# Kernel optimization log

Hardware: AMD Instinct MI355X
Metric: run time of the kernel (lower is better)

## Reference

```python
import jax, jax.numpy as jnp
import numpy as np

N = 4096
D = 256
TAU = 0.8
LAM = 0.5
K0, K1 = 64, 128


def setup_inputs() -> dict:
    key = jax.random.key(0)
    ks = jax.random.split(key, 20)
    s = 1.0 / np.sqrt(D)
    pos = (jax.random.uniform(ks[3], (N, N)) < 0.01).astype(jnp.float32)
    pos = pos.at[jnp.arange(N), jnp.arange(N)].set(1.0)  # guarantee a positive per row
    return {
        'z_mp': jax.random.normal(ks[0], (N, D), jnp.float32),
        'z_sc': jax.random.normal(ks[1], (N, D), jnp.float32),
        'feat': jax.random.normal(ks[2], (N, D), jnp.float32),
        'pos': pos,
        'im2c0': jax.random.randint(ks[4], (N,), 0, K0, jnp.int32),
        'im2c1': jax.random.randint(ks[5], (N,), 0, K1, jnp.int32),
        'centroids0': jax.random.normal(ks[6], (K0, D), jnp.float32),
        'centroids1': jax.random.normal(ks[7], (K1, D), jnp.float32),
        'density0': jax.random.uniform(ks[8], (K0,), jnp.float32) + 0.5,
        'density1': jax.random.uniform(ks[9], (K1,), jnp.float32) + 0.5,
        'pW1': jax.random.normal(ks[10], (D, D), jnp.float32) * s * 1.414,
        'pb1': jnp.zeros((D,), jnp.float32),
        'pW2': jax.random.normal(ks[11], (D, D), jnp.float32) * s * 1.414,
        'pb2': jnp.zeros((D,), jnp.float32),
        'mW1': jax.random.normal(ks[12], (D, D), jnp.float32) * s,
        'mb1': jnp.zeros((D,), jnp.float32),
        'mW2': jax.random.normal(ks[13], (D, D), jnp.float32) * s,
        'mb2': jnp.zeros((D,), jnp.float32),
    }


def _mlp(x, W1, b1, W2, b2):
    # nn.Linear -> ELU -> nn.Linear (torch Linear: x @ W.T + b)
    return jax.nn.elu(x @ W1.T + b1) @ W2.T + b2


def _sim(z1, z2, tau):
    n1 = jnp.linalg.norm(z1, axis=-1, keepdims=True)
    n2 = jnp.linalg.norm(z2, axis=-1, keepdims=True)
    return jnp.exp((z1 @ z2.T) / (n1 @ n2.T) / tau)


def _nce(sim_matrix, pos):
    m = sim_matrix / (sim_matrix.sum(axis=1, keepdims=True) + 1e-8)
    return -jnp.log((m * pos).sum(axis=-1)).mean()


def _pocl(z_anchor, z, im2cs, centroids, densities):
    n = z_anchor.shape[0]
    # weight[a,b] = #levels where a,b share a cluster (original: coo @ coo.T summed)
    sames = [(c[:, None] == c[None, :]).astype(z.dtype) for c in im2cs]
    weight = sames[0] + sames[1]
    node_prototypes = jnp.zeros_like(z)
    loss = jnp.float32(0.0)
    for same, im2c, protos, dens in zip(sames, im2cs, centroids, densities):
        # original aliases weight_clus = weight, so masking accumulates in-place
        weight = weight * same
        c = (weight @ z) / weight.sum(axis=1)[:, None]
        node_prototypes = node_prototypes + 0.1 * c
        phi = dens[im2c]
        pos_p = jnp.exp((z_anchor * node_prototypes).sum(axis=1) / phi)
        neg_p = jnp.exp((z_anchor @ protos.T) / dens).mean(axis=1) * n
        loss = loss + (-jnp.log(pos_p / neg_p)).mean()
    return loss / len(im2cs)


def reference(z_mp, z_sc, feat, pos, im2c0, im2c1, centroids0, centroids1,
              density0, density1, pW1, pb1, pW2, pb2, mW1, mb1, mW2, mb2):
    z_proj_mp = _mlp(z_mp, pW1, pb1, pW2, pb2)
    z_proj_sc = _mlp(z_sc, pW1, pb1, pW2, pb2)
    m_mp2sc = _sim(z_proj_mp, z_proj_sc, TAU)
    lori_mp = _nce(m_mp2sc, pos)
    lori_sc = _nce(m_mp2sc.T, pos)
    proto_loss = _pocl(z_sc, z_mp, [im2c0, im2c1],
                       [centroids0, centroids1], [density0, density1])
    mp_intra = _mlp(z_mp, mW1, mb1, mW2, mb2)
    loss_intramp = _nce(_sim(mp_intra, mp_intra, 0.05), pos)
    proj_mp_feat = _mlp(z_mp, pW1, pb1, pW2, pb2)
    proj_feat = _mlp(feat, pW1, pb1, pW2, pb2)
    lori_mpfeat = _nce(_sim(proj_mp_feat, proj_feat, TAU), pos)
    lori_featmp = _nce(_sim(proj_feat, proj_mp_feat, TAU), pos)
    return (LAM * lori_mp + (1 - LAM) * lori_sc + 0.3 * loss_intramp
            + proto_loss + 0.01 * lori_mpfeat + 0.01 * lori_featmp)
```

## Files before the change

### kernel.cpp

```cpp
#include <hip/hip_runtime.h>
#include <math.h>


#define NROWS 4096
#define DIM   256
#define ND    ((size_t)NROWS * DIM)

typedef unsigned short u16;
typedef unsigned int   u32;
typedef unsigned long long u64;
typedef __attribute__((ext_vector_type(8))) short bf16x8;
typedef __attribute__((ext_vector_type(4))) float f32x4;

__device__ __forceinline__ u16 f2bf(float f) {
    u32 u = __float_as_uint(f);
    return (u16)((u + 0x7fffu + ((u >> 16) & 1u)) >> 16);
}
__device__ __forceinline__ float bf2f(u16 h) {
    return __uint_as_float(((u32)h) << 16);
}

__device__ __forceinline__ void gload16(const u16* g, u16* l) {
    __builtin_amdgcn_global_load_lds(
        (const __attribute__((address_space(1))) u32*)g,
        (__attribute__((address_space(3))) u32*)l, 16, 0, 0);
}

template<int ROWS>
__device__ __forceinline__ void stage_panel(const u16* P, int kk, u16* S, int tid) {
#pragma unroll
    for (int p = 0; p < ROWS / 64; ++p) {
        const int ch = p * 256 + tid, row = ch >> 2, seg = ch & 3;
        gload16(P + (size_t)row * DIM + kk + seg * 8, &S[ch * 8]);
    }
}

__device__ __forceinline__ void wait_lgkm0() {
    asm volatile("s_waitcnt lgkmcnt(0)" ::: "memory");
    __builtin_amdgcn_sched_barrier(0);
}
template<int N> __device__ __forceinline__ void wait_vm() {
    if constexpr (N == 0)      asm volatile("s_waitcnt vmcnt(0)" ::: "memory");
    else if constexpr (N == 3) asm volatile("s_waitcnt vmcnt(3)" ::: "memory");
    else if constexpr (N == 4) asm volatile("s_waitcnt vmcnt(4)" ::: "memory");
}

__device__ __forceinline__ float rowsum16(float v) {
    v += __int_as_float(__builtin_amdgcn_update_dpp(0, __float_as_int(v), 0x118, 0xf, 0xf, true));
    v += __int_as_float(__builtin_amdgcn_update_dpp(0, __float_as_int(v), 0x114, 0xf, 0xf, true));
    v += __int_as_float(__builtin_amdgcn_update_dpp(0, __float_as_int(v), 0x112, 0xf, 0xf, true));
    v += __int_as_float(__builtin_amdgcn_update_dpp(0, __float_as_int(v), 0x111, 0xf, 0xf, true));
    return v;
}

struct PreArgs {
    const float* in0; const float* in1; const float* in2;
    const float* w0; const float* w1; const float* w2; const float* w3;
    const float* c0; const float* c1;
    const float* pos; const float* z_mp;
    const int* im0; const int* im1;
};
__global__ __launch_bounds__(256) void fused_pre(PreArgs p,
                                                 u16* __restrict__ INb,
                                                 u16* __restrict__ Wb,
                                                 u16* __restrict__ CB,
                                                 u64* __restrict__ bits,
                                                 float* __restrict__ S01,
                                                 float* __restrict__ cnt01)
{
    const int b = blockIdx.x, tid = threadIdx.x;
    if (b < 3072) {
        const int z = b >> 10;
        const float* s = z == 0 ? p.in0 : (z == 1 ? p.in1 : p.in2);
        const int i = (b & 1023) * 256 + tid;
        const float4 v = ((const float4*)s)[i];
        ushort4 o;
        o.x = f2bf(v.x); o.y = f2bf(v.y); o.z = f2bf(v.z); o.w = f2bf(v.w);
        ((ushort4*)(INb + (size_t)z * ND))[i] = o;
    } else if (b < 3328) {
        const int q = b - 3072, wi = q >> 6;
        const float* s = wi == 0 ? p.w0 : (wi == 1 ? p.w1 : (wi == 2 ? p.w2 : p.w3));
        const int i = (q & 63) * 256 + tid;
        const float4 v = ((const float4*)s)[i];
        ushort4 o;
        o.x = f2bf(v.x); o.y = f2bf(v.y); o.z = f2bf(v.z); o.w = f2bf(v.w);
        ((ushort4*)(Wb + (size_t)wi * 65536))[i] = o;
    } else if (b < 3376) {
        const int i = (b - 3328) * 256 + tid;
        const float4 v = (i < 4096) ? ((const float4*)p.c0)[i]
                                    : ((const float4*)p.c1)[i - 4096];
        ushort4 o;
        o.x = f2bf(v.x); o.y = f2bf(v.y); o.z = f2bf(v.z); o.w = f2bf(v.w);
        ((ushort4*)CB)[i] = o;
    } else if (b < 7472) {
        const int i = b - 3376;
        const int w = tid >> 6, l = tid & 63;
#pragma unroll
        for (int c = 0; c < 16; ++c) {
            const int j = c * 256 + w * 64 + l;
            const float v = p.pos[(size_t)i * NROWS + j];
            const u64 m = __ballot(v != 0.f);
            if (l == 0) bits[(size_t)i * 64 + c * 4 + w] = m;
        }
    } else {
        const int r = b - 7472;
        const int pp = p.im0[r] * 128 + p.im1[r];
        atomicAdd(&S01[(size_t)pp * DIM + tid], p.z_mp[(size_t)r * DIM + tid]);
        if (tid == 0) atomicAdd(&cnt01[pp], 1.f);
    }
}

template<int ACT, int REMAP, int SQ>
__device__ __forceinline__ void mlp_body(int bx, int by, u16* lds, int tid,
                                         const u16* __restrict__ IN,
                                         const u16* __restrict__ Wp,
                                         const u16* __restrict__ Wm,
                                         const float* __restrict__ bp,
                                         const float* __restrict__ bm,
                                         u16* __restrict__ OUT,
                                         float* __restrict__ SS)
{
    u16* As = lds;
    u16* Bs = lds + 3 * 2048;
    const bool intra = by >= 192;
    const int arow = (REMAP && intra) ? (by - 192) * 64 : by * 64;
    const u16* A = IN + (size_t)arow * DIM;
    const u16* B = (intra ? Wm : Wp) + (size_t)(bx * 128) * DIM;
    const float* bias = intra ? bm : bp;
    const int l = tid & 63, w = tid >> 6, wr = w >> 1, wc = w & 1;
    const int lr = l & 15, lk = l >> 4;

    f32x4 acc[2][4] = {};
    stage_panel<64>(A, 0, As, tid);
    stage_panel<128>(B, 0, Bs, tid);
    stage_panel<64>(A, 32, As + 2048, tid);
    stage_panel<128>(B, 32, Bs + 4096, tid);
    wait_vm<3>();
    __builtin_amdgcn_s_barrier();
#pragma unroll
    for (int t = 0; t < 8; ++t) {
        bf16x8 a[2], b[4];
#pragma unroll
        for (int mi = 0; mi < 2; ++mi)
            a[mi] = *(const bf16x8*)&As[(t % 3) * 2048 + (wr * 32 + mi * 16 + lr) * 32 + lk * 8];
#pragma unroll
        for (int ni = 0; ni < 4; ++ni)
            b[ni] = *(const bf16x8*)&Bs[(t % 3) * 4096 + (wc * 64 + ni * 16 + lr) * 32 + lk * 8];
        if (t < 6) {
            stage_panel<64>(A, (t + 2) * 32, As + ((t + 2) % 3) * 2048, tid);
            stage_panel<128>(B, (t + 2) * 32, Bs + ((t + 2) % 3) * 4096, tid);
        }
        wait_lgkm0();
#pragma unroll
        for (int mi = 0; mi < 2; ++mi)
#pragma unroll
            for (int ni = 0; ni < 4; ++ni)
                acc[mi][ni] = __builtin_amdgcn_mfma_f32_16x16x32_bf16(a[mi], b[ni], acc[mi][ni], 0, 0, 0);
        if (t < 6)      { wait_vm<3>(); __builtin_amdgcn_s_barrier(); }
        else if (t < 7) { wait_vm<0>(); __builtin_amdgcn_s_barrier(); }
    }

    const int j0 = bx * 128;
    float bv[4];
#pragma unroll
    for (int ni = 0; ni < 4; ++ni) bv[ni] = bias[j0 + wc * 64 + ni * 16 + lr];
#pragma unroll
    for (int mi = 0; mi < 2; ++mi)
#pragma unroll
        for (int r = 0; r < 4; ++r) {
            const int row = by * 64 + wr * 32 + mi * 16 + lk * 4 + r;
            float v4[4], sq = 0.f;
#pragma unroll
            for (int ni = 0; ni < 4; ++ni) {
                float v = acc[mi][ni][r] + bv[ni];
                if (ACT) v = v > 0.f ? v : expm1f(v);
                v4[ni] = v;
                sq += v * v;
            }
            if (SQ) {
                sq = rowsum16(sq);
                if (lr == 15) atomicAdd(&SS[row], sq);
            }
#pragma unroll
            for (int ni = 0; ni < 4; ++ni)
                OUT[(size_t)row * DIM + j0 + wc * 64 + ni * 16 + lr] = f2bf(v4[ni]);
        }
}

__device__ __forceinline__ void gcent_body(int bx, int by, u16* lds, int tid,
                                           const u16* __restrict__ Zb,
                                           const u16* __restrict__ CB,
                                           float* __restrict__ G)
{
    u16* As = lds;
    u16* Bs = lds + 3 * 4096;
    const int i0 = by * 128, j0 = bx * 64;
    const u16* A = Zb + (size_t)i0 * DIM;
    const u16* B = CB + (size_t)j0 * DIM;
    const int l = tid & 63, w = tid >> 6, wr = w >> 1, wc = w & 1;
    const int lr = l & 15, lk = l >> 4;

    f32x4 acc[4][2] = {};
    stage_panel<128>(A, 0, As, tid);
    stage_panel<64>(B, 0, Bs, tid);
    stage_panel<128>(A, 32, As + 4096, tid);
    stage_panel<64>(B, 32, Bs + 2048, tid);
    wait_vm<3>();
    __builtin_amdgcn_s_barrier();
#pragma unroll
    for (int t = 0; t < 8; ++t) {
        bf16x8 a[4], b[2];
#pragma unroll
        for (int mi = 0; mi < 4; ++mi)
            a[mi] = *(const bf16x8*)&As[(t % 3) * 4096 + (wr * 64 + mi * 16 + lr) * 32 + lk * 8];
#pragma unroll
        for (int ni = 0; ni < 2; ++ni)
            b[ni] = *(const bf16x8*)&Bs[(t % 3) * 2048 + (wc * 32 + ni * 16 + lr) * 32 + lk * 8];
        if (t < 6) {
            stage_panel<128>(A, (t + 2) * 32, As + ((t + 2) % 3) * 4096, tid);
            stage_panel<64>(B, (t + 2) * 32, Bs + ((t + 2) % 3) * 2048, tid);
        }
        wait_lgkm0();
#pragma unroll
        for (int mi = 0; mi < 4; ++mi)
#pragma unroll
            for (int ni = 0; ni < 2; ++ni)
                acc[mi][ni] = __builtin_amdgcn_mfma_f32_16x16x32_bf16(a[mi], b[ni], acc[mi][ni], 0, 0, 0);
        if (t < 6)      { wait_vm<3>(); __builtin_amdgcn_s_barrier(); }
        else if (t < 7) { wait_vm<0>(); __builtin_amdgcn_s_barrier(); }
    }

#pragma unroll
    for (int mi = 0; mi < 4; ++mi)
#pragma unroll
        for (int r = 0; r < 4; ++r) {
            const int row = i0 + wr * 64 + mi * 16 + lk * 4 + r;
#pragma unroll
            for (int ni = 0; ni < 2; ++ni)
                G[(size_t)row * 192 + j0 + wc * 32 + ni * 16 + lr] = acc[mi][ni][r];
        }
}

__device__ __forceinline__ void pocl_body(int blk, int tid,
                                          const float* __restrict__ z_sc,
                                          const int* __restrict__ i0a,
                                          const int* __restrict__ i1a,
                                          const float* __restrict__ S0,
                                          const float* __restrict__ S01,
                                          const float* __restrict__ cnt0,
                                          const float* __restrict__ cnt01,
                                          const float* __restrict__ G,
                                          const float* __restrict__ d0,
                                          const float* __restrict__ d1,
                                          float* __restrict__ L1,
                                          float* __restrict__ L2)
{
    const int w = tid >> 6, l = tid & 63;
    const int a = blk * 4 + w;
    const int k0 = i0a[a], k1 = i1a[a];
    const int p = k0 * 128 + k1;
    const float n0 = cnt0[k0], n01 = cnt01[p];
    const float inv1 = 1.f / (n0 + n01), inv2 = 1.f / n01;
    const float4 s0  = *(const float4*)&S0[(size_t)k0 * DIM + l * 4];
    const float4 s01 = *(const float4*)&S01[(size_t)p * DIM + l * 4];
    const float4 zd  = *(const float4*)&z_sc[(size_t)a * DIM + l * 4];

    float dot1 = 0.f, dot2 = 0.f;
    {
        const float c1x = (s0.x + s01.x) * inv1, c2x = s01.x * inv2;
        const float c1y = (s0.y + s01.y) * inv1, c2y = s01.y * inv2;
        const float c1z = (s0.z + s01.z) * inv1, c2z = s01.z * inv2;
        const float c1w = (s0.w + s01.w) * inv1, c2w = s01.w * inv2;
        dot1 = zd.x * c1x + zd.y * c1y + zd.z * c1z + zd.w * c1w;
        dot2 = zd.x * (c1x + c2x) + zd.y * (c1y + c2y) + zd.z * (c1z + c2z) + zd.w * (c1w + c2w);
    }
    dot1 *= 0.1f; dot2 *= 0.1f;
#pragma unroll
    for (int m = 1; m < 64; m <<= 1) {
        dot1 += __shfl_xor(dot1, m);
        dot2 += __shfl_xor(dot2, m);
    }

    const float x0 = G[(size_t)a * 192 + l] / d0[l];
    float M0 = x0;
#pragma unroll
    for (int m = 1; m < 64; m <<= 1) M0 = fmaxf(M0, __shfl_xor(M0, m));
    float e0 = __expf(x0 - M0);
#pragma unroll
    for (int m = 1; m < 64; m <<= 1) e0 += __shfl_xor(e0, m);

    const float x1a = G[(size_t)a * 192 + 64 + l] / d1[l];
    const float x1b = G[(size_t)a * 192 + 128 + l] / d1[64 + l];
    float M1 = fmaxf(x1a, x1b);
#pragma unroll
    for (int m = 1; m < 64; m <<= 1) M1 = fmaxf(M1, __shfl_xor(M1, m));
    float e1 = __expf(x1a - M1) + __expf(x1b - M1);
#pragma unroll
    for (int m = 1; m < 64; m <<= 1) e1 += __shfl_xor(e1, m);

    if (l == 0) {
        const float lneg1 = M0 + logf(e0) - logf(64.f)  + logf(4096.f);
        const float lneg2 = M1 + logf(e1) - logf(128.f) + logf(4096.f);
        L1[a] = lneg1 - dot1 / d0[k0];
        L2[a] = lneg2 - dot2 / d1[k1];
    }
}

struct C1Args {
    const u16* INb; const u16* Wb; const u16* CB;
    const float* pb1; const float* mb1;
    u16* Hb; float* G;
    const float* S01; const float* cnt01; float* S0; float* cnt0;
};
__global__ __launch_bounds__(256, 4) void combo1(C1Args a)
{
    extern __shared__ u16 smem[];
    const int b = blockIdx.x, tid = threadIdx.x;
    if (b < 512) {
        mlp_body<1, 1, 0>(b & 1, b >> 1, smem, tid, a.INb, a.Wb, a.Wb + 2 * 65536,
                          a.pb1, a.mb1, a.Hb, nullptr);
    } else if (b < 608) {
        const int q = b - 512;
        gcent_body(q % 3, q / 3, smem, tid, a.INb + ND, a.CB, a.G);
    } else {
        const int k0 = b - 608, d = tid;
        float s = 0.f;
        for (int k1 = 0; k1 < 128; ++k1)
            s += a.S01[(size_t)(k0 * 128 + k1) * DIM + d];
        a.S0[(size_t)k0 * DIM + d] = s;
        float* c = (float*)smem;
        if (d < 128) c[d] = a.cnt01[k0 * 128 + d];
        __syncthreads();
        if (d == 0) {
            float t = 0.f;
            for (int i = 0; i < 128; ++i) t += c[i];
            a.cnt0[k0] = t;
        }
    }
}

struct C2Args {
    const u16* Hb; const u16* Wb;
    const float* pb2; const float* mb2;
    u16* PROJ; float* SS;
    const float* z_sc; const int* im0; const int* im1;
    const float* S0; const float* S01; const float* cnt0; const float* cnt01;
    const float* G; const float* d0; const float* d1;
    float* L1; float* L2;
};
__global__ __launch_bounds__(256, 4) void combo2(C2Args a)
{
    extern __shared__ u16 smem[];
    const int b = blockIdx.x, tid = threadIdx.x;
    if (b < 512) {
        mlp_body<0, 0, 1>(b & 1, b >> 1, smem, tid, a.Hb, a.Wb + 65536,
                          a.Wb + 3 * 65536, a.pb2, a.mb2, a.PROJ, a.SS);
    } else {
        pocl_body(b - 512, tid, a.z_sc, a.im0, a.im1, a.S0, a.S01, a.cnt0,
                  a.cnt01, a.G, a.d0, a.d1, a.L1, a.L2);
    }
}

__global__ __launch_bounds__(256, 3) void simstat3c(const u16* __restrict__ PROJ,
                                                    const u64* __restrict__ bits,
                                                    const float* __restrict__ SS,
                                                    float* __restrict__ ST)
{
    const int bid = blockIdx.x;
    int z, by, bx;
    if (bid < 1024) {
        z = 0;
        const int x = bid & 7, j = bid >> 3;
        by = (x >> 1) * 8 + (j >> 4);
        bx = (x & 1) * 16 + (j & 15);
    } else if (bid < 1552) {
        z = 1;
        const int u = bid - 1024;
        const int t = (u & 7) * 66 + (u >> 3);
        int r = (int)((65.0f - sqrtf(4225.0f - 8.0f * (float)t)) * 0.5f);
        int off = 32 * r - (r * (r - 1)) / 2;
        if (t < off)                   { --r; off -= 33 - r; }
        else if (t >= off + (32 - r))  { off += 32 - r; ++r; }
        by = r; bx = r + (t - off);
    } else {
        z = 2;
        const int v = bid - 1552;
        const int x = v & 7, j = v >> 3;
        by = (x >> 1) * 8 + (j >> 4);
        bx = (x & 1) * 16 + (j & 15);
    }

    __shared__ __align__(16) u16 As[3][128 * 32];
    __shared__ __align__(16) u16 Bs[3][128 * 32];
    const int tid = threadIdx.x;
    int ao, bo;
    float* rsr; float* rsc;
    switch (z) {
        case 0:  ao = 0; bo = 1; rsr = ST + 0;     rsc = ST + 8192;  break;
        case 1:  ao = 3; bo = 3; rsr = ST + 16384; rsc = ST + 16384; break;
        default: ao = 0; bo = 2; rsr = ST + 24576; rsc = ST + 32768; break;
    }
    const float invtau = (z == 1) ? 20.f : 1.25f;
    const bool docol = (z != 1) || (bx > by);
    const int i0 = by * 128, j0 = bx * 128;
    const u16* A = PROJ + (size_t)ao * ND + (size_t)i0 * DIM;
    const u16* B = PROJ + (size_t)bo * ND + (size_t)j0 * DIM;
    const int l = tid & 63, w = tid >> 6, wr = w >> 1, wc = w & 1;
    const int lr = l & 15, lk = l >> 4;

    f32x4 acc[4][4] = {};
    stage_panel<128>(A, 0, As[0], tid);
    stage_panel<128>(B, 0, Bs[0], tid);
    stage_panel<128>(A, 32, As[1], tid);
    stage_panel<128>(B, 32, Bs[1], tid);
    wait_vm<4>();
    __builtin_amdgcn_s_barrier();
#pragma unroll
    for (int t = 0; t < 8; ++t) {
        bf16x8 a[4], b[4];
#pragma unroll
        for (int mi = 0; mi < 4; ++mi)
            a[mi] = *(const bf16x8*)&As[t % 3][(wr * 64 + mi * 16 + lr) * 32 + lk * 8];
#pragma unroll
        for (int ni = 0; ni < 4; ++ni)
            b[ni] = *(const bf16x8*)&Bs[t % 3][(wc * 64 + ni * 16 + lr) * 32 + lk * 8];
        if (t < 6) {
            stage_panel<128>(A, (t + 2) * 32, As[(t + 2) % 3], tid);
            stage_panel<128>(B, (t + 2) * 32, Bs[(t + 2) % 3], tid);
        }
        wait_lgkm0();
#pragma unroll
        for (int mi = 0; mi < 4; ++mi)
#pragma unroll
            for (int ni = 0; ni < 4; ++ni)
                acc[mi][ni] = __builtin_amdgcn_mfma_f32_16x16x32_bf16(a[mi], b[ni], acc[mi][ni], 0, 0, 0);
        if (t < 6)      { wait_vm<4>(); __builtin_amdgcn_s_barrier(); }
        else if (t < 7) { wait_vm<0>(); __builtin_amdgcn_s_barrier(); }
    }

    const float* ssa = SS + ao * 4096;
    const float* ssb = SS + bo * 4096;
    float ri[4][4], rj[4];
#pragma unroll
    for (int mi = 0; mi < 4; ++mi)
#pragma unroll
        for (int r = 0; r < 4; ++r)
            ri[mi][r] = rsqrtf(ssa[i0 + wr * 64 + mi * 16 + lk * 4 + r]) * invtau;
#pragma unroll
    for (int ni = 0; ni < 4; ++ni)
        rj[ni] = rsqrtf(ssb[j0 + wc * 64 + ni * 16 + lr]);
#pragma unroll
    for (int mi = 0; mi < 4; ++mi)
#pragma unroll
        for (int ni = 0; ni < 4; ++ni)
#pragma unroll
            for (int r = 0; r < 4; ++r)
                acc[mi][ni][r] = __expf(acc[mi][ni][r] * ri[mi][r] * rj[ni]);

#pragma unroll
    for (int mi = 0; mi < 4; ++mi)
#pragma unroll
        for (int r = 0; r < 4; ++r) {
            const int i = i0 + wr * 64 + mi * 16 + lk * 4 + r;
            const u64 pw = bits[(size_t)i * 64 + bx * 2 + wc];
            float rsum = 0.f, psum = 0.f;
#pragma unroll
            for (int ni = 0; ni < 4; ++ni) {
                const float ev = acc[mi][ni][r];
                rsum += ev;
                psum += ((pw >> (ni * 16 + lr)) & 1ull) ? ev : 0.f;
            }
            rsum = rowsum16(rsum);
            psum = rowsum16(psum);
            if (lr == 15) {
                atomicAdd(&rsr[i], rsum);
                atomicAdd(&rsr[4096 + i], psum);
            }
        }

    if (docol) {
#pragma unroll
        for (int ni = 0; ni < 4; ++ni) {
            const int j = j0 + wc * 64 + ni * 16 + lr;
            const u64 pw = bits[(size_t)j * 64 + by * 2 + wr];
            float csum = 0.f, qsum = 0.f;
#pragma unroll
            for (int mi = 0; mi < 4; ++mi)
#pragma unroll
                for (int r = 0; r < 4; ++r) {
                    const float ev = acc[mi][ni][r];
                    csum += ev;
                    qsum += ((pw >> (mi * 16 + lk * 4 + r)) & 1ull) ? ev : 0.f;
                }
            csum += __shfl_xor(csum, 16); csum += __shfl_xor(csum, 32);
            qsum += __shfl_xor(qsum, 16); qsum += __shfl_xor(qsum, 32);
            if (lk == 0) {
                atomicAdd(&rsc[j], csum);
                atomicAdd(&rsc[4096 + j], qsum);
            }
        }
    }
}

__global__ __launch_bounds__(256) void final_reduce(const float* __restrict__ st,
                                                    const float* __restrict__ L1,
                                                    const float* __restrict__ L2,
                                                    float* __restrict__ out)
{
    const int t = threadIdx.x;
    const float* rs0 = st + 0;      const float* pr0 = st + 4096;
    const float* rs1 = st + 8192;   const float* pr1 = st + 12288;
    const float* rs2 = st + 16384;  const float* pr2 = st + 20480;
    const float* rs3 = st + 24576;  const float* pr3 = st + 28672;
    const float* rs4 = st + 32768;  const float* pr4 = st + 36864;

    float acc = 0.f;
    for (int i = t; i < NROWS; i += 256) {
        const float lmp = logf(rs0[i] + 1e-8f) - logf(pr0[i]);
        const float lsc = logf(rs1[i] + 1e-8f) - logf(pr1[i]);
        const float lin = logf(rs2[i] + 1e-8f) - logf(pr2[i]);
        const float lmf = logf(rs3[i] + 1e-8f) - logf(pr3[i]);
        const float lfm = logf(rs4[i] + 1e-8f) - logf(pr4[i]);
        acc += 0.5f * (lmp + lsc) + 0.3f * lin
             + 0.01f * (lmf + lfm) + 0.5f * (L1[i] + L2[i]);
    }
    __shared__ float red[256];
    red[t] = acc; __syncthreads();
    for (int s = 128; s > 0; s >>= 1) {
        if (t < s) red[t] += red[t + s];
        __syncthreads();
    }
    if (t == 0) out[0] = red[0] * (1.f / 4096.f);
}

extern "C" void kernel_launch(void* const* d_in, const int* in_sizes, int n_in,
                              void* d_out, int out_size, void* d_ws, size_t ws_size,
                              hipStream_t stream)
{
    const float* z_mp = (const float*)d_in[0];
    const float* z_sc = (const float*)d_in[1];
    const float* feat = (const float*)d_in[2];
    const float* pos  = (const float*)d_in[3];
    const int*   im0  = (const int*)d_in[4];
    const int*   im1  = (const int*)d_in[5];
    const float* c0   = (const float*)d_in[6];
    const float* c1   = (const float*)d_in[7];
    const float* d0   = (const float*)d_in[8];
    const float* d1   = (const float*)d_in[9];
    const float* pW1  = (const float*)d_in[10];
    const float* pb1  = (const float*)d_in[11];
    const float* pW2  = (const float*)d_in[12];
    const float* pb2  = (const float*)d_in[13];
    const float* mW1  = (const float*)d_in[14];
    const float* mb1  = (const float*)d_in[15];
    const float* mW2  = (const float*)d_in[16];
    const float* mb2  = (const float*)d_in[17];
    float* out = (float*)d_out;
    float* ws  = (float*)d_ws;
    (void)in_sizes; (void)n_in; (void)out_size; (void)ws_size;

    float* ST   = ws;
    float* S0f  = ST + 40960;
    float* CN0  = S0f + 16384;
    float* CN01 = CN0 + 64;
    float* S01f = CN01 + 8192;
    float* SS   = S01f + (size_t)8192 * DIM;
    float* ZEND = SS + 16384;
    float* G    = ZEND;
    float* L1   = G + (size_t)NROWS * 192;
    float* L2   = L1 + NROWS;
    u64*  bits  = (u64*)(L2 + NROWS);
    u16*  INb   = (u16*)(bits + (size_t)NROWS * 64);
    u16*  Hb    = INb + 3 * ND;
    u16*  PROJ  = Hb + 4 * ND;
    u16*  Wb    = PROJ + 4 * ND;
    u16*  CB    = Wb + 4 * 65536;

    hipMemsetAsync(ws, 0, (size_t)(ZEND - ws) * sizeof(float), stream);

    const dim3 blk(256);
    const size_t lds_bytes = 36 * 1024;

    PreArgs pa{z_mp, z_sc, feat, pW1, pW2, mW1, mW2, c0, c1, pos, z_mp, im0, im1};
    fused_pre<<<11568, blk, 0, stream>>>(pa, INb, Wb, CB, bits, S01f, CN01);

    C1Args a1{INb, Wb, CB, pb1, mb1, Hb, G, S01f, CN01, S0f, CN0};
    combo1<<<672, blk, lds_bytes, stream>>>(a1);

    C2Args a2{Hb, Wb, pb2, mb2, PROJ, SS, z_sc, im0, im1,
              S0f, S01f, CN0, CN01, G, d0, d1, L1, L2};
    combo2<<<1536, blk, lds_bytes, stream>>>(a2);

    simstat3c<<<2576, blk, 0, stream>>>(PROJ, bits, SS, ST);

    final_reduce<<<1, blk, 0, stream>>>(ST, L1, L2, out);
}
```

Before: 140.9 us.

## Store projections as fp8 and run similarity GEMMs with fp8 MFMA

```diff
diff --git a/kernel.cpp b/kernel.cpp
--- a/kernel.cpp
+++ b/kernel.cpp
@@ -6,6 +6,7 @@
 #define DIM   256
 #define ND    ((size_t)NROWS * DIM)
 
+typedef unsigned char  u8;
 typedef unsigned short u16;
 typedef unsigned int   u32;
 typedef unsigned long long u64;
@@ -19,8 +20,12 @@
 __device__ __forceinline__ float bf2f(u16 h) {
     return __uint_as_float(((u32)h) << 16);
 }
-
-__device__ __forceinline__ void gload16(const u16* g, u16* l) {
+__device__ __forceinline__ u8 f2fp8(float v) {
+    const int r = __builtin_amdgcn_cvt_pk_fp8_f32(v, 0.f, 0, false);
+    return (u8)(r & 0xff);
+}
+
+__device__ __forceinline__ void gload16(const void* g, void* l) {
     __builtin_amdgcn_global_load_lds(
         (const __attribute__((address_space(1))) u32*)g,
         (__attribute__((address_space(3))) u32*)l, 16, 0, 0);
@@ -32,6 +37,13 @@
     for (int p = 0; p < ROWS / 64; ++p) {
         const int ch = p * 256 + tid, row = ch >> 2, seg = ch & 3;
         gload16(P + (size_t)row * DIM + kk + seg * 8, &S[ch * 8]);
+    }
+}
+__device__ __forceinline__ void stage_panel8(const u8* P, int kk, u8* S, int tid) {
+#pragma unroll
+    for (int p = 0; p < 2; ++p) {
+        const int ch = p * 256 + tid, row = ch >> 2, seg = ch & 3;
+        gload16(P + (size_t)row * DIM + kk + seg * 16, S + ch * 16);
     }
 }
 
@@ -110,14 +122,14 @@
     }
 }
 
-template<int ACT, int REMAP, int SQ>
+template<int ACT, int REMAP, int SQ, int F8>
 __device__ __forceinline__ void mlp_body(int bx, int by, u16* lds, int tid,
                                          const u16* __restrict__ IN,
                                          const u16* __restrict__ Wp,
                                          const u16* __restrict__ Wm,
                                          const float* __restrict__ bp,
                                          const float* __restrict__ bm,
-                                         u16* __restrict__ OUT,
+                                         void* __restrict__ OUT,
                                          float* __restrict__ SS)
 {
     u16* As = lds;
@@ -182,8 +194,11 @@
                 if (lr == 15) atomicAdd(&SS[row], sq);
             }
 #pragma unroll
-            for (int ni = 0; ni < 4; ++ni)
-                OUT[(size_t)row * DIM + j0 + wc * 64 + ni * 16 + lr] = f2bf(v4[ni]);
+            for (int ni = 0; ni < 4; ++ni) {
+                const size_t off = (size_t)row * DIM + j0 + wc * 64 + ni * 16 + lr;
+                if (F8) ((u8*)OUT)[off]  = f2fp8(v4[ni]);
+                else    ((u16*)OUT)[off] = f2bf(v4[ni]);
+            }
         }
 }
 
@@ -317,8 +332,8 @@
     extern __shared__ u16 smem[];
     const int b = blockIdx.x, tid = threadIdx.x;
     if (b < 512) {
-        mlp_body<1, 1, 0>(b & 1, b >> 1, smem, tid, a.INb, a.Wb, a.Wb + 2 * 65536,
-                          a.pb1, a.mb1, a.Hb, nullptr);
+        mlp_body<1, 1, 0, 0>(b & 1, b >> 1, smem, tid, a.INb, a.Wb, a.Wb + 2 * 65536,
+                             a.pb1, a.mb1, a.Hb, nullptr);
     } else if (b < 608) {
         const int q = b - 512;
         gcent_body(q % 3, q / 3, smem, tid, a.INb + ND, a.CB, a.G);
@@ -342,7 +357,7 @@
 struct C2Args {
     const u16* Hb; const u16* Wb;
     const float* pb2; const float* mb2;
-    u16* PROJ; float* SS;
+    u8* PROJ8; float* SS;
     const float* z_sc; const int* im0; const int* im1;
     const float* S0; const float* S01; const float* cnt0; const float* cnt01;
     const float* G; const float* d0; const float* d1;
@@ -353,15 +368,15 @@
     extern __shared__ u16 smem[];
     const int b = blockIdx.x, tid = threadIdx.x;
     if (b < 512) {
-        mlp_body<0, 0, 1>(b & 1, b >> 1, smem, tid, a.Hb, a.Wb + 65536,
-                          a.Wb + 3 * 65536, a.pb2, a.mb2, a.PROJ, a.SS);
+        mlp_body<0, 0, 1, 1>(b & 1, b >> 1, smem, tid, a.Hb, a.Wb + 65536,
+                             a.Wb + 3 * 65536, a.pb2, a.mb2, a.PROJ8, a.SS);
     } else {
         pocl_body(b - 512, tid, a.z_sc, a.im0, a.im1, a.S0, a.S01, a.cnt0,
                   a.cnt01, a.G, a.d0, a.d1, a.L1, a.L2);
     }
 }
 
-__global__ __launch_bounds__(256, 3) void simstat3c(const u16* __restrict__ PROJ,
+__global__ __launch_bounds__(256, 3) void simstat3c(const u8* __restrict__ PROJ,
                                                     const u64* __restrict__ bits,
                                                     const float* __restrict__ SS,
                                                     float* __restrict__ ST)
@@ -390,8 +405,8 @@
         bx = (x & 1) * 16 + (j & 15);
     }
 
-    __shared__ __align__(16) u16 As[3][128 * 32];
-    __shared__ __align__(16) u16 Bs[3][128 * 32];
+    __shared__ __align__(16) u8 As[3][128 * 64];
+    __shared__ __align__(16) u8 Bs[3][128 * 64];
     const int tid = threadIdx.x;
     int ao, bo;
     float* rsr; float* rsc;
@@ -403,39 +418,45 @@
     const float invtau = (z == 1) ? 20.f : 1.25f;
     const bool docol = (z != 1) || (bx > by);
     const int i0 = by * 128, j0 = bx * 128;
-    const u16* A = PROJ + (size_t)ao * ND + (size_t)i0 * DIM;
-    const u16* B = PROJ + (size_t)bo * ND + (size_t)j0 * DIM;
+    const u8* A = PROJ + (size_t)ao * ND + (size_t)i0 * DIM;
+    const u8* B = PROJ + (size_t)bo * ND + (size_t)j0 * DIM;
     const int l = tid & 63, w = tid >> 6, wr = w >> 1, wc = w & 1;
     const int lr = l & 15, lk = l >> 4;
 
     f32x4 acc[4][4] = {};
-    stage_panel<128>(A, 0, As[0], tid);
-    stage_panel<128>(B, 0, Bs[0], tid);
-    stage_panel<128>(A, 32, As[1], tid);
-    stage_panel<128>(B, 32, Bs[1], tid);
+    stage_panel8(A, 0, As[0], tid);
+    stage_panel8(B, 0, Bs[0], tid);
+    stage_panel8(A, 64, As[1], tid);
+    stage_panel8(B, 64, Bs[1], tid);
     wait_vm<4>();
     __builtin_amdgcn_s_barrier();
 #pragma unroll
-    for (int t = 0; t < 8; ++t) {
-        bf16x8 a[4], b[4];
+    for (int t = 0; t < 4; ++t) {
+        long a[4][2], b[4][2];
 #pragma unroll
         for (int mi = 0; mi < 4; ++mi)
-            a[mi] = *(const bf16x8*)&As[t % 3][(wr * 64 + mi * 16 + lr) * 32 + lk * 8];
+#pragma unroll
+            for (int s = 0; s < 2; ++s)
+                a[mi][s] = *(const long*)&As[t % 3][(wr * 64 + mi * 16 + lr) * 64 + s * 32 + lk * 8];
 #pragma unroll
         for (int ni = 0; ni < 4; ++ni)
-            b[ni] = *(const bf16x8*)&Bs[t % 3][(wc * 64 + ni * 16 + lr) * 32 + lk * 8];
-        if (t < 6) {
-            stage_panel<128>(A, (t + 2) * 32, As[(t + 2) % 3], tid);
-            stage_panel<128>(B, (t + 2) * 32, Bs[(t + 2) % 3], tid);
+#pragma unroll
+            for (int s = 0; s < 2; ++s)
+                b[ni][s] = *(const long*)&Bs[t % 3][(wc * 64 + ni * 16 + lr) * 64 + s * 32 + lk * 8];
+        if (t < 2) {
+            stage_panel8(A, (t + 2) * 64, As[(t + 2) % 3], tid);
+            stage_panel8(B, (t + 2) * 64, Bs[(t + 2) % 3], tid);
         }
         wait_lgkm0();
 #pragma unroll
         for (int mi = 0; mi < 4; ++mi)
 #pragma unroll
-            for (int ni = 0; ni < 4; ++ni)
-                acc[mi][ni] = __builtin_amdgcn_mfma_f32_16x16x32_bf16(a[mi], b[ni], acc[mi][ni], 0, 0, 0);
-        if (t < 6)      { wait_vm<4>(); __builtin_amdgcn_s_barrier(); }
-        else if (t < 7) { wait_vm<0>(); __builtin_amdgcn_s_barrier(); }
+            for (int ni = 0; ni < 4; ++ni) {
+                acc[mi][ni] = __builtin_amdgcn_mfma_f32_16x16x32_fp8_fp8(a[mi][0], b[ni][0], acc[mi][ni], 0, 0, 0);
+                acc[mi][ni] = __builtin_amdgcn_mfma_f32_16x16x32_fp8_fp8(a[mi][1], b[ni][1], acc[mi][ni], 0, 0, 0);
+            }
+        if (t < 2)      { wait_vm<4>(); __builtin_amdgcn_s_barrier(); }
+        else if (t < 3) { wait_vm<0>(); __builtin_amdgcn_s_barrier(); }
     }
 
     const float* ssa = SS + ao * 4096;
@@ -572,8 +593,8 @@
     u64*  bits  = (u64*)(L2 + NROWS);
     u16*  INb   = (u16*)(bits + (size_t)NROWS * 64);
     u16*  Hb    = INb + 3 * ND;
-    u16*  PROJ  = Hb + 4 * ND;
-    u16*  Wb    = PROJ + 4 * ND;
+    u8*   PROJ8 = (u8*)(Hb + 4 * ND);
+    u16*  Wb    = (u16*)(PROJ8 + 4 * ND);
     u16*  CB    = Wb + 4 * 65536;
 
     hipMemsetAsync(ws, 0, (size_t)(ZEND - ws) * sizeof(float), stream);
@@ -587,11 +608,11 @@
     C1Args a1{INb, Wb, CB, pb1, mb1, Hb, G, S01f, CN01, S0f, CN0};
     combo1<<<672, blk, lds_bytes, stream>>>(a1);
 
-    C2Args a2{Hb, Wb, pb2, mb2, PROJ, SS, z_sc, im0, im1,
+    C2Args a2{Hb, Wb, pb2, mb2, PROJ8, SS, z_sc, im0, im1,
               S0f, S01f, CN0, CN01, G, d0, d1, L1, L2};
     combo2<<<1536, blk, lds_bytes, stream>>>(a2);
 
-    simstat3c<<<2576, blk, 0, stream>>>(PROJ, bits, SS, ST);
+    simstat3c<<<2576, blk, 0, stream>>>(PROJ8, bits, SS, ST);
 
     final_reduce<<<1, blk, 0, stream>>>(ST, L1, L2, out);
 }
```

New measurement: 145.9 us. 1.04x slower.

## Make similarity-stat kernel persistent and prefetch next tile during epilogue

Applied to the files above, without the earlier changes.

```diff
diff --git a/kernel.cpp b/kernel.cpp
--- a/kernel.cpp
+++ b/kernel.cpp
@@ -361,12 +361,16 @@
     }
 }
 
-__global__ __launch_bounds__(256, 3) void simstat3c(const u16* __restrict__ PROJ,
-                                                    const u64* __restrict__ bits,
-                                                    const float* __restrict__ SS,
-                                                    float* __restrict__ ST)
-{
-    const int bid = blockIdx.x;
+struct STile {
+    const u16* A; const u16* B;
+    const float* ssa; const float* ssb;
+    float* rsr; float* rsc;
+    float invtau;
+    int i0, j0, docol;
+};
+__device__ __forceinline__ STile decode_tile(int bid, const u16* PROJ,
+                                             const float* SS, float* ST)
+{
     int z, by, bx;
     if (bid < 1024) {
         z = 0;
@@ -389,116 +393,144 @@
         by = (x >> 1) * 8 + (j >> 4);
         bx = (x & 1) * 16 + (j & 15);
     }
-
-    __shared__ __align__(16) u16 As[3][128 * 32];
-    __shared__ __align__(16) u16 Bs[3][128 * 32];
-    const int tid = threadIdx.x;
-    int ao, bo;
-    float* rsr; float* rsc;
+    int ao, bo; float* rsr; float* rsc;
     switch (z) {
         case 0:  ao = 0; bo = 1; rsr = ST + 0;     rsc = ST + 8192;  break;
         case 1:  ao = 3; bo = 3; rsr = ST + 16384; rsc = ST + 16384; break;
         default: ao = 0; bo = 2; rsr = ST + 24576; rsc = ST + 32768; break;
     }
-    const float invtau = (z == 1) ? 20.f : 1.25f;
-    const bool docol = (z != 1) || (bx > by);
-    const int i0 = by * 128, j0 = bx * 128;
-    const u16* A = PROJ + (size_t)ao * ND + (size_t)i0 * DIM;
-    const u16* B = PROJ + (size_t)bo * ND + (size_t)j0 * DIM;
+    STile s;
+    s.i0 = by * 128; s.j0 = bx * 128;
+    s.A = PROJ + (size_t)ao * ND + (size_t)s.i0 * DIM;
+    s.B = PROJ + (size_t)bo * ND + (size_t)s.j0 * DIM;
+    s.ssa = SS + ao * 4096; s.ssb = SS + bo * 4096;
+    s.rsr = rsr; s.rsc = rsc;
+    s.invtau = (z == 1) ? 20.f : 1.25f;
+    s.docol = (z != 1) || (bx > by);
+    return s;
+}
+
+__global__ __launch_bounds__(256, 3) void simstat3p(const u16* __restrict__ PROJ,
+                                                    const u64* __restrict__ bits,
+                                                    const float* __restrict__ SS,
+                                                    float* __restrict__ ST)
+{
+    __shared__ __align__(16) u16 As[3][128 * 32];
+    __shared__ __align__(16) u16 Bs[3][128 * 32];
+    const int tid = threadIdx.x;
     const int l = tid & 63, w = tid >> 6, wr = w >> 1, wc = w & 1;
     const int lr = l & 15, lk = l >> 4;
-
-    f32x4 acc[4][4] = {};
-    stage_panel<128>(A, 0, As[0], tid);
-    stage_panel<128>(B, 0, Bs[0], tid);
-    stage_panel<128>(A, 32, As[1], tid);
-    stage_panel<128>(B, 32, Bs[1], tid);
+    const int blk = blockIdx.x;
+    const int nt = (blk < 272) ? 4 : 3;
+
+    STile cur = decode_tile(blk, PROJ, SS, ST);
+    stage_panel<128>(cur.A, 0, As[0], tid);
+    stage_panel<128>(cur.B, 0, Bs[0], tid);
+    stage_panel<128>(cur.A, 32, As[1], tid);
+    stage_panel<128>(cur.B, 32, Bs[1], tid);
     wait_vm<4>();
     __builtin_amdgcn_s_barrier();
-#pragma unroll
-    for (int t = 0; t < 8; ++t) {
-        bf16x8 a[4], b[4];
+
+    int phase = 0;
+    for (int ti = 0; ti < nt; ++ti) {
+        const bool lastt = (ti == nt - 1);
+        STile nxt = cur;
+        if (!lastt) nxt = decode_tile(blk + 768 * (ti + 1), PROJ, SS, ST);
+
+        f32x4 acc[4][4] = {};
+#pragma unroll
+        for (int t = 0; t < 8; ++t) {
+            const int bi = (phase + t) % 3;
+            bf16x8 a[4], b[4];
+#pragma unroll
+            for (int mi = 0; mi < 4; ++mi)
+                a[mi] = *(const bf16x8*)&As[bi][(wr * 64 + mi * 16 + lr) * 32 + lk * 8];
+#pragma unroll
+            for (int ni = 0; ni < 4; ++ni)
+                b[ni] = *(const bf16x8*)&Bs[bi][(wc * 64 + ni * 16 + lr) * 32 + lk * 8];
+            if (t < 6) {
+                const int bs = (phase + t + 2) % 3;
+                stage_panel<128>(cur.A, (t + 2) * 32, As[bs], tid);
+                stage_panel<128>(cur.B, (t + 2) * 32, Bs[bs], tid);
+            } else if (!lastt) {
+                const int bs = (phase + t + 2) % 3;
+                stage_panel<128>(nxt.A, (t - 6) * 32, As[bs], tid);
+                stage_panel<128>(nxt.B, (t - 6) * 32, Bs[bs], tid);
+            }
+            wait_lgkm0();
+#pragma unroll
+            for (int mi = 0; mi < 4; ++mi)
+#pragma unroll
+                for (int ni = 0; ni < 4; ++ni)
+                    acc[mi][ni] = __builtin_amdgcn_mfma_f32_16x16x32_bf16(a[mi], b[ni], acc[mi][ni], 0, 0, 0);
+            if (!lastt)      { wait_vm<4>(); __builtin_amdgcn_s_barrier(); }
+            else if (t < 6)  { wait_vm<4>(); __builtin_amdgcn_s_barrier(); }
+            else if (t == 6) { wait_vm<0>(); __builtin_amdgcn_s_barrier(); }
+        }
+
+        float ri[4][4], rj[4];
 #pragma unroll
         for (int mi = 0; mi < 4; ++mi)
-            a[mi] = *(const bf16x8*)&As[t % 3][(wr * 64 + mi * 16 + lr) * 32 + lk * 8];
+#pragma unroll
+            for (int r = 0; r < 4; ++r)
+                ri[mi][r] = rsqrtf(cur.ssa[cur.i0 + wr * 64 + mi * 16 + lk * 4 + r]) * cur.invtau;
 #pragma unroll
         for (int ni = 0; ni < 4; ++ni)
-            b[ni] = *(const bf16x8*)&Bs[t % 3][(wc * 64 + ni * 16 + lr) * 32 + lk * 8];
-        if (t < 6) {
-            stage_panel<128>(A, (t + 2) * 32, As[(t + 2) % 3], tid);
-            stage_panel<128>(B, (t + 2) * 32, Bs[(t + 2) % 3], tid);
-        }
-        wait_lgkm0();
+            rj[ni] = rsqrtf(cur.ssb[cur.j0 + wc * 64 + ni * 16 + lr]);
 #pragma unroll
         for (int mi = 0; mi < 4; ++mi)
 #pragma unroll
             for (int ni = 0; ni < 4; ++ni)
-                acc[mi][ni] = __builtin_amdgcn_mfma_f32_16x16x32_bf16(a[mi], b[ni], acc[mi][ni], 0, 0, 0);
-        if (t < 6)      { wait_vm<4>(); __builtin_amdgcn_s_barrier(); }
-        else if (t < 7) { wait_vm<0>(); __builtin_amdgcn_s_barrier(); }
-    }
-
-    const float* ssa = SS + ao * 4096;
-    const float* ssb = SS + bo * 4096;
-    float ri[4][4], rj[4];
-#pragma unroll
-    for (int mi = 0; mi < 4; ++mi)
-#pragma unroll
-        for (int r = 0; r < 4; ++r)
-            ri[mi][r] = rsqrtf(ssa[i0 + wr * 64 + mi * 16 + lk * 4 + r]) * invtau;
-#pragma unroll
-    for (int ni = 0; ni < 4; ++ni)
-        rj[ni] = rsqrtf(ssb[j0 + wc * 64 + ni * 16 + lr]);
-#pragma unroll
-    for (int mi = 0; mi < 4; ++mi)
-#pragma unroll
-        for (int ni = 0; ni < 4; ++ni)
-#pragma unroll
-            for (int r = 0; r < 4; ++r)
-                acc[mi][ni][r] = __expf(acc[mi][ni][r] * ri[mi][r] * rj[ni]);
-
-#pragma unroll
-    for (int mi = 0; mi < 4; ++mi)
-#pragma unroll
-        for (int r = 0; r < 4; ++r) {
-            const int i = i0 + wr * 64 + mi * 16 + lk * 4 + r;
-            const u64 pw = bits[(size_t)i * 64 + bx * 2 + wc];
-            float rsum = 0.f, psum = 0.f;
+#pragma unroll
+                for (int r = 0; r < 4; ++r)
+                    acc[mi][ni][r] = __expf(acc[mi][ni][r] * ri[mi][r] * rj[ni]);
+
+        const int jw = cur.j0 >> 6, iw = cur.i0 >> 6;
+#pragma unroll
+        for (int mi = 0; mi < 4; ++mi)
+#pragma unroll
+            for (int r = 0; r < 4; ++r) {
+                const int i = cur.i0 + wr * 64 + mi * 16 + lk * 4 + r;
+                const u64 pw = bits[(size_t)i * 64 + jw + wc];
+                float rsum = 0.f, psum = 0.f;
+#pragma unroll
+                for (int ni = 0; ni < 4; ++ni) {
+                    const float ev = acc[mi][ni][r];
+                    rsum += ev;
+                    psum += ((pw >> (ni * 16 + lr)) & 1ull) ? ev : 0.f;
+                }
+                rsum = rowsum16(rsum);
+                psum = rowsum16(psum);
+                if (lr == 15) {
+                    atomicAdd(&cur.rsr[i], rsum);
+                    atomicAdd(&cur.rsr[4096 + i], psum);
+                }
+            }
+        if (cur.docol) {
 #pragma unroll
             for (int ni = 0; ni < 4; ++ni) {
-                const float ev = acc[mi][ni][r];
-                rsum += ev;
-                psum += ((pw >> (ni * 16 + lr)) & 1ull) ? ev : 0.f;
+                const int j = cur.j0 + wc * 64 + ni * 16 + lr;
+                const u64 pw = bits[(size_t)j * 64 + iw + wr];
+                float csum = 0.f, qsum = 0.f;
+#pragma unroll
+                for (int mi = 0; mi < 4; ++mi)
+#pragma unroll
+                    for (int r = 0; r < 4; ++r) {
+                        const float ev = acc[mi][ni][r];
+                        csum += ev;
+                        qsum += ((pw >> (mi * 16 + lk * 4 + r)) & 1ull) ? ev : 0.f;
+                    }
+                csum += __shfl_xor(csum, 16); csum += __shfl_xor(csum, 32);
+                qsum += __shfl_xor(qsum, 16); qsum += __shfl_xor(qsum, 32);
+                if (lk == 0) {
+                    atomicAdd(&cur.rsc[j], csum);
+                    atomicAdd(&cur.rsc[4096 + j], qsum);
+                }
             }
-            rsum = rowsum16(rsum);
-            psum = rowsum16(psum);
-            if (lr == 15) {
-                atomicAdd(&rsr[i], rsum);
-                atomicAdd(&rsr[4096 + i], psum);
-            }
-        }
-
-    if (docol) {
-#pragma unroll
-        for (int ni = 0; ni < 4; ++ni) {
-            const int j = j0 + wc * 64 + ni * 16 + lr;
-            const u64 pw = bits[(size_t)j * 64 + by * 2 + wr];
-            float csum = 0.f, qsum = 0.f;
-#pragma unroll
-            for (int mi = 0; mi < 4; ++mi)
-#pragma unroll
-                for (int r = 0; r < 4; ++r) {
-                    const float ev = acc[mi][ni][r];
-                    csum += ev;
-                    qsum += ((pw >> (mi * 16 + lk * 4 + r)) & 1ull) ? ev : 0.f;
-                }
-            csum += __shfl_xor(csum, 16); csum += __shfl_xor(csum, 32);
-            qsum += __shfl_xor(qsum, 16); qsum += __shfl_xor(qsum, 32);
-            if (lk == 0) {
-                atomicAdd(&rsc[j], csum);
-                atomicAdd(&rsc[4096 + j], qsum);
-            }
-        }
+        }
+
+        phase = (phase + 2) % 3;
+        cur = nxt;
     }
 }
 
@@ -591,7 +623,7 @@
               S0f, S01f, CN0, CN01, G, d0, d1, L1, L2};
     combo2<<<1536, blk, lds_bytes, stream>>>(a2);
 
-    simstat3c<<<2576, blk, 0, stream>>>(PROJ, bits, SS, ST);
+    simstat3p<<<768, blk, 0, stream>>>(PROJ, bits, SS, ST);
 
     final_reduce<<<1, blk, 0, stream>>>(ST, L1, L2, out);
 }
```

Result: faster. 136.4 us (-3.2%).
